# Kernel tuning notes

Hardware: AMD Instinct MI355X
Metric: run time of the kernel (lower is better)

The kernel has to match this reference:

```python
import jax, jax.numpy as jnp
import numpy as np

N = 10000   # nodes
E = 160000  # edges (avg degree 16)
IN = 512
HID = 512
OUT = 512


def setup_inputs() -> dict:
    key = jax.random.key(0)
    ks = jax.random.split(key, 8)
    x = jax.random.normal(ks[0], (N, IN), dtype=jnp.float32)
    edge_index = jax.random.randint(ks[1], (2, E), 0, N, dtype=jnp.int64)
    def w(k, fi, fo):
        return jax.random.normal(k, (fi, fo), dtype=jnp.float32) * (1.0 / np.sqrt(fi)).astype(np.float32)
    return {
        "x": x,
        "edge_index": edge_index,
        "W1": w(ks[2], IN, HID), "b1": jnp.zeros((HID,), jnp.float32),
        "W2": w(ks[3], HID, HID), "b2": jnp.zeros((HID,), jnp.float32),
        "W3": w(ks[4], HID, OUT), "b3": jnp.zeros((OUT,), jnp.float32),
    }


def _gcn_norm(edge_index, n):
    # add self loops, then symmetric normalization D^{-1/2} (A+I) D^{-1/2}
    loops = jnp.arange(n, dtype=edge_index.dtype)
    row = jnp.concatenate([edge_index[0], loops])  # source
    col = jnp.concatenate([edge_index[1], loops])  # target (aggregation dim)
    deg = jax.ops.segment_sum(jnp.ones_like(col, jnp.float32), col, num_segments=n)
    dis = jnp.where(deg > 0, jax.lax.rsqrt(jnp.maximum(deg, 1.0)), 0.0)
    norm = dis[row] * dis[col]  # [E+N]
    return row, col, norm


def _gcn_layer(x, row, col, norm, W, b, n):
    h = x @ W                                    # [N, d_out] dense GEMM
    msg = h[row] * norm[:, None]                 # gather + scale, [E+N, d_out]
    out = jax.ops.segment_sum(msg, col, num_segments=n)  # scatter-add
    return out + b


def reference(x, edge_index, W1, b1, W2, b2, W3, b3):
    n = x.shape[0]
    row, col, norm = _gcn_norm(edge_index, n)
    h = _gcn_layer(x, row, col, norm, W1, b1, n)
    h = jax.nn.relu(h)  # dropout is identity in eval mode
    h = _gcn_layer(h, row, col, norm, W2, b2, n)
    h = jax.nn.relu(h)
    h = _gcn_layer(h, row, col, norm, W3, b3, n)
    return h
```

## Files before the change

kernel.cpp:

```cpp
#include <hip/hip_runtime.h>

typedef __attribute__((ext_vector_type(8))) short bf16x8;
typedef __attribute__((ext_vector_type(4))) float f32x4;

#define N_NODES 10000
#define N_EDGES 160000
#define FDIM    512
#define ELL     64
#define BM 64
#define BN 128
#define BK 64
#define TM 157
#define NGEMM (TM * 4)
#define NSCAT 625
#define NTRAN 768

__device__ __forceinline__ float bf2f(unsigned int u) {
    union { unsigned int i; float f; } v; v.i = u << 16; return v.f;
}
__device__ __forceinline__ float bfs2f(short s) {
    return bf2f((unsigned int)(unsigned short)s);
}
__device__ __forceinline__ unsigned short f2bf(float f) {
    union { float f; unsigned int u; } v; v.f = f;
    unsigned int u = v.u;
    unsigned int r = u + 0x7fffu + ((u >> 16) & 1u);
    return (unsigned short)(r >> 16);
}
__device__ __forceinline__ void gload_lds16(const void* g, void* l) {
    __builtin_amdgcn_global_load_lds(
        (const __attribute__((address_space(1))) unsigned int*)g,
        (__attribute__((address_space(3))) unsigned int*)l, 16, 0, 0);
}
__device__ __forceinline__ int wave_is_f32(const unsigned int* w) {
    unsigned int v = w[(size_t)(threadIdx.x & 63) * 1000];
    unsigned int ex = (v >> 7) & 0xFFu;
    unsigned long long inb = __ballot(ex >= 100u && ex <= 140u);
    return (__popcll(inb) >= 48) ? 0 : 1;
}

__global__ __launch_bounds__(256) void prep_v6(
        const void* __restrict__ x, const void* __restrict__ ei,
        const void* __restrict__ W1, const void* __restrict__ W2,
        const void* __restrict__ W3, unsigned short* __restrict__ Wt,
        int* __restrict__ cnt, int* __restrict__ flags) {
    int b = blockIdx.x;
    if (b < NTRAN) {
        __shared__ unsigned short tile[32][33];
        int z = b >> 8, t = b & 255;
        const void* W = (z == 0) ? W1 : (z == 1) ? W2 : W3;
        unsigned short* out = Wt + (size_t)z * FDIM * FDIM;
        int ff32 = wave_is_f32((const unsigned int*)W);
        int tx = threadIdx.x & 31, ty = threadIdx.x >> 5;
        int xcol = (t & 15) * 32 + tx;
        int y0 = (t >> 4) * 32 + ty;
        #pragma unroll
        for (int j = 0; j < 32; j += 8) {
            int idx = (y0 + j) * FDIM + xcol;
            unsigned short v = ff32 ? f2bf(((const float*)W)[idx])
                                    : ((const unsigned short*)W)[idx];
            tile[ty + j][tx] = v;
        }
        __syncthreads();
        int x2 = (t >> 4) * 32 + tx;
        int y2 = (t & 15) * 32 + ty;
        #pragma unroll
        for (int j = 0; j < 32; j += 8)
            out[(y2 + j) * FDIM + x2] = tile[tx][ty + j];
    } else if (b < NTRAN + NSCAT) {
        const unsigned long long* e64 = (const unsigned long long*)ei;
        unsigned long long v = e64[(size_t)(threadIdx.x & 63) * 2500];
        unsigned long long big = __ballot(v > 0xFFFFFFFFull);
        int i64 = (big == 0ull);
        int e = (b - NTRAN) * 256 + threadIdx.x;
        int c = i64 ? (int)((const long long*)ei)[N_EDGES + e]
                    : ((const int*)ei)[N_EDGES + e];
        atomicAdd(&cnt[c], 1);
    } else {
        if (threadIdx.x < 64) {
            const unsigned long long* e64 = (const unsigned long long*)ei;
            unsigned long long v = e64[(size_t)threadIdx.x * 2500];
            unsigned long long big = __ballot(v > 0xFFFFFFFFull);
            const unsigned int* xw = (const unsigned int*)x;
            unsigned int w = xw[(size_t)threadIdx.x * 1000];
            unsigned int ex = (w >> 7) & 0xFFu;
            unsigned long long inb = __ballot(ex >= 100u && ex <= 140u);
            if (threadIdx.x == 0) {
                flags[0] = (big == 0ull) ? 1 : 0;
                flags[1] = (__popcll(inb) >= 48) ? 0 : 1;
            }
        }
    }
}

__global__ __launch_bounds__(256) void gemm_scat_v6(
        const void* __restrict__ Ap, const unsigned short* __restrict__ Bt,
        unsigned short* __restrict__ C, int M, int a_ext,
        const int* __restrict__ flags, const void* __restrict__ ei,
        const int* __restrict__ cnt, int* __restrict__ cursor,
        int2* __restrict__ ell, int do_scatter) {
    __shared__ unsigned short As[BM * BK];
    __shared__ unsigned short Bs[BN * BK];
    if (do_scatter && blockIdx.x >= NGEMM) {
        int e = (blockIdx.x - NGEMM) * 256 + threadIdx.x;
        if (e < N_EDGES) {
            int r, c;
            if (flags[0]) {
                r = (int)((const long long*)ei)[e];
                c = (int)((const long long*)ei)[N_EDGES + e];
            } else {
                r = ((const int*)ei)[e];
                c = ((const int*)ei)[N_EDGES + e];
            }
            int slot = atomicAdd(&cursor[c], 1);
            if (slot < ELL) {
                float nrm = rsqrtf((float)((cnt[r] + 1) * (cnt[c] + 1)));
                int2 pr; pr.x = r; pr.y = __float_as_int(nrm);
                ell[(size_t)c * ELL + slot] = pr;
            }
        }
        return;
    }
    const int K = FDIM;
    const int af32 = a_ext ? flags[1] : 0;
    const int tid = threadIdx.x;
    const int t = blockIdx.x;
    const int bm = (t % TM) * BM, bn = (t / TM) * BN;
    const int lane = tid & 63, wv = tid >> 6;
    const int wm = (wv >> 1) * 32, wn = (wv & 1) * 64;
    const int lrow = lane & 15, lk = (lane >> 4) * 8;
    const unsigned short* Abf = (const unsigned short*)Ap;
    f32x4 acc[2][4] = {};

    for (int k0 = 0; k0 < K; k0 += BK) {
        if (!af32) {
            #pragma unroll
            for (int j = 0; j < 2; ++j) {
                int r0 = wv * 16 + j * 8;
                int arow = bm + r0 + (lane >> 3);
                if (arow >= M) arow = M - 1;
                gload_lds16(Abf + (size_t)arow * K + k0 + (lane & 7) * 8,
                            &As[r0 * BK]);
            }
            #pragma unroll
            for (int j = 0; j < 4; ++j) {
                int r0 = wv * 32 + j * 8;
                gload_lds16(Bt + (size_t)(bn + r0 + (lane >> 3)) * K + k0 + (lane & 7) * 8,
                            &Bs[r0 * BK]);
            }
        } else {
            #pragma unroll
            for (int j = 0; j < 4; ++j) {
                int r0 = wv * 32 + j * 8;
                gload_lds16(Bt + (size_t)(bn + r0 + (lane >> 3)) * K + k0 + (lane & 7) * 8,
                            &Bs[r0 * BK]);
            }
            #pragma unroll
            for (int i = 0; i < 2; ++i) {
                int c = tid + i * 256;
                int row = c >> 3, seg = (c & 7) * 8;
                int grow = bm + row;
                bf16x8 va = {};
                if (grow < M) {
                    const float* Af = (const float*)Ap + (size_t)grow * K + k0 + seg;
                    f32x4 lo = *(const f32x4*)Af;
                    f32x4 hi = *(const f32x4*)(Af + 4);
                    #pragma unroll
                    for (int jj = 0; jj < 4; ++jj) {
                        va[jj]     = (short)f2bf(lo[jj]);
                        va[4 + jj] = (short)f2bf(hi[jj]);
                    }
                }
                *(bf16x8*)(&As[row * BK + seg]) = va;
            }
        }
        __syncthreads();
        #pragma unroll
        for (int half = 0; half < 2; ++half) {
            bf16x8 af[2], bfr[4];
            #pragma unroll
            for (int f = 0; f < 2; ++f)
                af[f] = *(const bf16x8*)(&As[(wm + f * 16 + lrow) * BK + half * 32 + lk]);
            #pragma unroll
            for (int f = 0; f < 4; ++f)
                bfr[f] = *(const bf16x8*)(&Bs[(wn + f * 16 + lrow) * BK + half * 32 + lk]);
            #pragma unroll
            for (int fm = 0; fm < 2; ++fm)
                #pragma unroll
                for (int fn = 0; fn < 4; ++fn)
                    acc[fm][fn] = __builtin_amdgcn_mfma_f32_16x16x32_bf16(
                        af[fm], bfr[fn], acc[fm][fn], 0, 0, 0);
        }
        __syncthreads();
    }

    int crow = (lane >> 4) * 4;
    int ccol = lane & 15;
    #pragma unroll
    for (int fm = 0; fm < 2; ++fm) {
        #pragma unroll
        for (int fn = 0; fn < 4; ++fn) {
            #pragma unroll
            for (int r = 0; r < 4; ++r) {
                int row = bm + wm + fm * 16 + crow + r;
                if (row < M)
                    C[(size_t)row * FDIM + bn + wn + fn * 16 + ccol] =
                        f2bf(acc[fm][fn][r]);
            }
        }
    }
}

__global__ __launch_bounds__(256) void agg_v6(
        const unsigned short* __restrict__ g, const void* __restrict__ bias,
        const int* __restrict__ cnt, const int2* __restrict__ ell,
        void* __restrict__ out, int relu, int out_ext,
        const int* __restrict__ flags) {
    int wv = threadIdx.x >> 6, lane = threadIdx.x & 63;
    int i = blockIdx.x * 2 + (wv >> 1);
    int f = (wv & 1) * 256 + lane * 4;
    float a0 = 0.f, a1 = 0.f, a2 = 0.f, a3 = 0.f;
    int ci = cnt[i];
    int rows = (ci > ELL) ? ELL : ci;
    const int2* ep = ell + (size_t)i * ELL;
    int j = 0;
    for (; j + 4 <= rows; j += 4) {
        int2 p0 = ep[j], p1 = ep[j + 1], p2 = ep[j + 2], p3 = ep[j + 3];
        uint2 v0 = *(const uint2*)(g + (size_t)p0.x * FDIM + f);
        uint2 v1 = *(const uint2*)(g + (size_t)p1.x * FDIM + f);
        uint2 v2 = *(const uint2*)(g + (size_t)p2.x * FDIM + f);
        uint2 v3 = *(const uint2*)(g + (size_t)p3.x * FDIM + f);
        float w0 = __int_as_float(p0.y), w1 = __int_as_float(p1.y);
        float w2 = __int_as_float(p2.y), w3 = __int_as_float(p3.y);
        a0 += w0 * bf2f(v0.x & 0xffffu); a1 += w0 * bf2f(v0.x >> 16);
        a2 += w0 * bf2f(v0.y & 0xffffu); a3 += w0 * bf2f(v0.y >> 16);
        a0 += w1 * bf2f(v1.x & 0xffffu); a1 += w1 * bf2f(v1.x >> 16);
        a2 += w1 * bf2f(v1.y & 0xffffu); a3 += w1 * bf2f(v1.y >> 16);
        a0 += w2 * bf2f(v2.x & 0xffffu); a1 += w2 * bf2f(v2.x >> 16);
        a2 += w2 * bf2f(v2.y & 0xffffu); a3 += w2 * bf2f(v2.y >> 16);
        a0 += w3 * bf2f(v3.x & 0xffffu); a1 += w3 * bf2f(v3.x >> 16);
        a2 += w3 * bf2f(v3.y & 0xffffu); a3 += w3 * bf2f(v3.y >> 16);
    }
    for (; j < rows; ++j) {
        int2 pp = ep[j];
        float w = __int_as_float(pp.y);
        uint2 v = *(const uint2*)(g + (size_t)pp.x * FDIM + f);
        a0 += w * bf2f(v.x & 0xffffu); a1 += w * bf2f(v.x >> 16);
        a2 += w * bf2f(v.y & 0xffffu); a3 += w * bf2f(v.y >> 16);
    }
    float wself = 1.0f / (float)(ci + 1);
    uint2 vs = *(const uint2*)(g + (size_t)i * FDIM + f);
    a0 += wself * bf2f(vs.x & 0xffffu); a1 += wself * bf2f(vs.x >> 16);
    a2 += wself * bf2f(vs.y & 0xffffu); a3 += wself * bf2f(vs.y >> 16);
    int ff32 = flags[1];
    if (ff32) {
        f32x4 bb = *(const f32x4*)((const float*)bias + f);
        a0 += bb[0]; a1 += bb[1]; a2 += bb[2]; a3 += bb[3];
    } else {
        uint2 bb = *(const uint2*)((const unsigned short*)bias + f);
        a0 += bf2f(bb.x & 0xffffu); a1 += bf2f(bb.x >> 16);
        a2 += bf2f(bb.y & 0xffffu); a3 += bf2f(bb.y >> 16);
    }
    if (relu) {
        a0 = fmaxf(a0, 0.f); a1 = fmaxf(a1, 0.f);
        a2 = fmaxf(a2, 0.f); a3 = fmaxf(a3, 0.f);
    }
    if (out_ext && ff32) {
        f32x4 o = {a0, a1, a2, a3};
        *(f32x4*)((float*)out + (size_t)i * FDIM + f) = o;
    } else {
        uint2 o;
        o.x = (unsigned int)f2bf(a0) | ((unsigned int)f2bf(a1) << 16);
        o.y = (unsigned int)f2bf(a2) | ((unsigned int)f2bf(a3) << 16);
        *(uint2*)((unsigned short*)out + (size_t)i * FDIM + f) = o;
    }
}

extern "C" void kernel_launch(void* const* d_in, const int* in_sizes, int n_in,
                              void* d_out, int out_size, void* d_ws, size_t ws_size,
                              hipStream_t stream) {
    (void)in_sizes; (void)n_in; (void)out_size; (void)ws_size;
    const void* x  = d_in[0];
    const void* ei = d_in[1];
    const void* W1 = d_in[2];
    const void* b1 = d_in[3];
    const void* W2 = d_in[4];
    const void* b2 = d_in[5];
    const void* W3 = d_in[6];
    const void* b3 = d_in[7];

    char* p = (char*)d_ws;
    auto alloc = [&](size_t bytes) -> void* {
        void* r = (void*)p;
        p += (bytes + 255) & ~(size_t)255;
        return r;
    };
    int*  flags   = (int*) alloc(16);
    int*  cntcur  = (int*) alloc((size_t)2 * N_NODES * 4);
    int2* ell     = (int2*)alloc((size_t)N_NODES * ELL * 8);
    unsigned short* Wt = (unsigned short*)alloc((size_t)3 * FDIM * FDIM * 2);
    unsigned short* g  = (unsigned short*)alloc((size_t)N_NODES * FDIM * 2);
    int* cnt    = cntcur;
    int* cursor = cntcur + N_NODES;
    unsigned short* Wt1 = Wt;
    unsigned short* Wt2 = Wt + (size_t)FDIM * FDIM;
    unsigned short* Wt3 = Wt + (size_t)2 * FDIM * FDIM;
    unsigned short* h   = (unsigned short*)d_out;

    hipMemsetAsync(cntcur, 0, (size_t)2 * N_NODES * 4, stream);
    prep_v6<<<NTRAN + NSCAT + 1, 256, 0, stream>>>(x, ei, W1, W2, W3, Wt, cnt, flags);

    gemm_scat_v6<<<NGEMM + NSCAT, 256, 0, stream>>>(x, Wt1, g, N_NODES, 1, flags,
                                                    ei, cnt, cursor, ell, 1);
    agg_v6<<<N_NODES / 2, 256, 0, stream>>>(g, b1, cnt, ell, h, 1, 0, flags);
    gemm_scat_v6<<<NGEMM, 256, 0, stream>>>(h, Wt2, g, N_NODES, 0, flags,
                                            ei, cnt, cursor, ell, 0);
    agg_v6<<<N_NODES / 2, 256, 0, stream>>>(g, b2, cnt, ell, h, 1, 0, flags);
    gemm_scat_v6<<<NGEMM, 256, 0, stream>>>(h, Wt3, g, N_NODES, 0, flags,
                                            ei, cnt, cursor, ell, 0);
    agg_v6<<<N_NODES / 2, 256, 0, stream>>>(g, b3, cnt, ell, d_out, 0, 1, flags);
}
```

Baseline: 226.4 us.

## Fuse all GCN phases into one persistent cooperative kernel with grid syncs

```diff
diff --git a/kernel.cpp b/kernel.cpp
--- a/kernel.cpp
+++ b/kernel.cpp
@@ -1,4 +1,7 @@
 #include <hip/hip_runtime.h>
+#include <hip/hip_cooperative_groups.h>
+
+namespace cg = cooperative_groups;
 
 typedef __attribute__((ext_vector_type(8))) short bf16x8;
 typedef __attribute__((ext_vector_type(4))) float f32x4;
@@ -14,12 +17,10 @@
 #define NGEMM (TM * 4)
 #define NSCAT 625
 #define NTRAN 768
+#define BLK 256
 
 __device__ __forceinline__ float bf2f(unsigned int u) {
     union { unsigned int i; float f; } v; v.i = u << 16; return v.f;
-}
-__device__ __forceinline__ float bfs2f(short s) {
-    return bf2f((unsigned int)(unsigned short)s);
 }
 __device__ __forceinline__ unsigned short f2bf(float f) {
     union { float f; unsigned int u; } v; v.f = f;
@@ -39,94 +40,12 @@
     return (__popcll(inb) >= 48) ? 0 : 1;
 }
 
-__global__ __launch_bounds__(256) void prep_v6(
-        const void* __restrict__ x, const void* __restrict__ ei,
-        const void* __restrict__ W1, const void* __restrict__ W2,
-        const void* __restrict__ W3, unsigned short* __restrict__ Wt,
-        int* __restrict__ cnt, int* __restrict__ flags) {
-    int b = blockIdx.x;
-    if (b < NTRAN) {
-        __shared__ unsigned short tile[32][33];
-        int z = b >> 8, t = b & 255;
-        const void* W = (z == 0) ? W1 : (z == 1) ? W2 : W3;
-        unsigned short* out = Wt + (size_t)z * FDIM * FDIM;
-        int ff32 = wave_is_f32((const unsigned int*)W);
-        int tx = threadIdx.x & 31, ty = threadIdx.x >> 5;
-        int xcol = (t & 15) * 32 + tx;
-        int y0 = (t >> 4) * 32 + ty;
-        #pragma unroll
-        for (int j = 0; j < 32; j += 8) {
-            int idx = (y0 + j) * FDIM + xcol;
-            unsigned short v = ff32 ? f2bf(((const float*)W)[idx])
-                                    : ((const unsigned short*)W)[idx];
-            tile[ty + j][tx] = v;
-        }
-        __syncthreads();
-        int x2 = (t >> 4) * 32 + tx;
-        int y2 = (t & 15) * 32 + ty;
-        #pragma unroll
-        for (int j = 0; j < 32; j += 8)
-            out[(y2 + j) * FDIM + x2] = tile[tx][ty + j];
-    } else if (b < NTRAN + NSCAT) {
-        const unsigned long long* e64 = (const unsigned long long*)ei;
-        unsigned long long v = e64[(size_t)(threadIdx.x & 63) * 2500];
-        unsigned long long big = __ballot(v > 0xFFFFFFFFull);
-        int i64 = (big == 0ull);
-        int e = (b - NTRAN) * 256 + threadIdx.x;
-        int c = i64 ? (int)((const long long*)ei)[N_EDGES + e]
-                    : ((const int*)ei)[N_EDGES + e];
-        atomicAdd(&cnt[c], 1);
-    } else {
-        if (threadIdx.x < 64) {
-            const unsigned long long* e64 = (const unsigned long long*)ei;
-            unsigned long long v = e64[(size_t)threadIdx.x * 2500];
-            unsigned long long big = __ballot(v > 0xFFFFFFFFull);
-            const unsigned int* xw = (const unsigned int*)x;
-            unsigned int w = xw[(size_t)threadIdx.x * 1000];
-            unsigned int ex = (w >> 7) & 0xFFu;
-            unsigned long long inb = __ballot(ex >= 100u && ex <= 140u);
-            if (threadIdx.x == 0) {
-                flags[0] = (big == 0ull) ? 1 : 0;
-                flags[1] = (__popcll(inb) >= 48) ? 0 : 1;
-            }
-        }
-    }
-}
-
-__global__ __launch_bounds__(256) void gemm_scat_v6(
-        const void* __restrict__ Ap, const unsigned short* __restrict__ Bt,
-        unsigned short* __restrict__ C, int M, int a_ext,
-        const int* __restrict__ flags, const void* __restrict__ ei,
-        const int* __restrict__ cnt, int* __restrict__ cursor,
-        int2* __restrict__ ell, int do_scatter) {
-    __shared__ unsigned short As[BM * BK];
-    __shared__ unsigned short Bs[BN * BK];
-    if (do_scatter && blockIdx.x >= NGEMM) {
-        int e = (blockIdx.x - NGEMM) * 256 + threadIdx.x;
-        if (e < N_EDGES) {
-            int r, c;
-            if (flags[0]) {
-                r = (int)((const long long*)ei)[e];
-                c = (int)((const long long*)ei)[N_EDGES + e];
-            } else {
-                r = ((const int*)ei)[e];
-                c = ((const int*)ei)[N_EDGES + e];
-            }
-            int slot = atomicAdd(&cursor[c], 1);
-            if (slot < ELL) {
-                float nrm = rsqrtf((float)((cnt[r] + 1) * (cnt[c] + 1)));
-                int2 pr; pr.x = r; pr.y = __float_as_int(nrm);
-                ell[(size_t)c * ELL + slot] = pr;
-            }
-        }
-        return;
-    }
+__device__ __forceinline__ void gemm_tile(
+        const void* Ap, const unsigned short* Bt, unsigned short* C,
+        int M, int af32, int item, unsigned short* As, unsigned short* Bs,
+        int tid, int lane, int wv) {
     const int K = FDIM;
-    const int af32 = a_ext ? flags[1] : 0;
-    const int tid = threadIdx.x;
-    const int t = blockIdx.x;
-    const int bm = (t % TM) * BM, bn = (t / TM) * BN;
-    const int lane = tid & 63, wv = tid >> 6;
+    const int bm = (item % TM) * BM, bn = (item / TM) * BN;
     const int wm = (wv >> 1) * 32, wn = (wv & 1) * 64;
     const int lrow = lane & 15, lk = (lane >> 4) * 8;
     const unsigned short* Abf = (const unsigned short*)Ap;
@@ -197,9 +116,9 @@
     int crow = (lane >> 4) * 4;
     int ccol = lane & 15;
     #pragma unroll
-    for (int fm = 0; fm < 2; ++fm) {
+    for (int fm = 0; fm < 2; ++fm)
         #pragma unroll
-        for (int fn = 0; fn < 4; ++fn) {
+        for (int fn = 0; fn < 4; ++fn)
             #pragma unroll
             for (int r = 0; r < 4; ++r) {
                 int row = bm + wm + fm * 16 + crow + r;
@@ -207,73 +126,186 @@
                     C[(size_t)row * FDIM + bn + wn + fn * 16 + ccol] =
                         f2bf(acc[fm][fn][r]);
             }
-        }
-    }
-}
-
-__global__ __launch_bounds__(256) void agg_v6(
-        const unsigned short* __restrict__ g, const void* __restrict__ bias,
-        const int* __restrict__ cnt, const int2* __restrict__ ell,
-        void* __restrict__ out, int relu, int out_ext,
-        const int* __restrict__ flags) {
-    int wv = threadIdx.x >> 6, lane = threadIdx.x & 63;
-    int i = blockIdx.x * 2 + (wv >> 1);
-    int f = (wv & 1) * 256 + lane * 4;
-    float a0 = 0.f, a1 = 0.f, a2 = 0.f, a3 = 0.f;
-    int ci = cnt[i];
-    int rows = (ci > ELL) ? ELL : ci;
-    const int2* ep = ell + (size_t)i * ELL;
-    int j = 0;
-    for (; j + 4 <= rows; j += 4) {
-        int2 p0 = ep[j], p1 = ep[j + 1], p2 = ep[j + 2], p3 = ep[j + 3];
-        uint2 v0 = *(const uint2*)(g + (size_t)p0.x * FDIM + f);
-        uint2 v1 = *(const uint2*)(g + (size_t)p1.x * FDIM + f);
-        uint2 v2 = *(const uint2*)(g + (size_t)p2.x * FDIM + f);
-        uint2 v3 = *(const uint2*)(g + (size_t)p3.x * FDIM + f);
-        float w0 = __int_as_float(p0.y), w1 = __int_as_float(p1.y);
-        float w2 = __int_as_float(p2.y), w3 = __int_as_float(p3.y);
-        a0 += w0 * bf2f(v0.x & 0xffffu); a1 += w0 * bf2f(v0.x >> 16);
-        a2 += w0 * bf2f(v0.y & 0xffffu); a3 += w0 * bf2f(v0.y >> 16);
-        a0 += w1 * bf2f(v1.x & 0xffffu); a1 += w1 * bf2f(v1.x >> 16);
-        a2 += w1 * bf2f(v1.y & 0xffffu); a3 += w1 * bf2f(v1.y >> 16);
-        a0 += w2 * bf2f(v2.x & 0xffffu); a1 += w2 * bf2f(v2.x >> 16);
-        a2 += w2 * bf2f(v2.y & 0xffffu); a3 += w2 * bf2f(v2.y >> 16);
-        a0 += w3 * bf2f(v3.x & 0xffffu); a1 += w3 * bf2f(v3.x >> 16);
-        a2 += w3 * bf2f(v3.y & 0xffffu); a3 += w3 * bf2f(v3.y >> 16);
-    }
-    for (; j < rows; ++j) {
-        int2 pp = ep[j];
-        float w = __int_as_float(pp.y);
-        uint2 v = *(const uint2*)(g + (size_t)pp.x * FDIM + f);
-        a0 += w * bf2f(v.x & 0xffffu); a1 += w * bf2f(v.x >> 16);
-        a2 += w * bf2f(v.y & 0xffffu); a3 += w * bf2f(v.y >> 16);
-    }
-    float wself = 1.0f / (float)(ci + 1);
-    uint2 vs = *(const uint2*)(g + (size_t)i * FDIM + f);
-    a0 += wself * bf2f(vs.x & 0xffffu); a1 += wself * bf2f(vs.x >> 16);
-    a2 += wself * bf2f(vs.y & 0xffffu); a3 += wself * bf2f(vs.y >> 16);
-    int ff32 = flags[1];
-    if (ff32) {
-        f32x4 bb = *(const f32x4*)((const float*)bias + f);
-        a0 += bb[0]; a1 += bb[1]; a2 += bb[2]; a3 += bb[3];
-    } else {
-        uint2 bb = *(const uint2*)((const unsigned short*)bias + f);
-        a0 += bf2f(bb.x & 0xffffu); a1 += bf2f(bb.x >> 16);
-        a2 += bf2f(bb.y & 0xffffu); a3 += bf2f(bb.y >> 16);
-    }
-    if (relu) {
-        a0 = fmaxf(a0, 0.f); a1 = fmaxf(a1, 0.f);
-        a2 = fmaxf(a2, 0.f); a3 = fmaxf(a3, 0.f);
-    }
-    if (out_ext && ff32) {
-        f32x4 o = {a0, a1, a2, a3};
-        *(f32x4*)((float*)out + (size_t)i * FDIM + f) = o;
-    } else {
-        uint2 o;
-        o.x = (unsigned int)f2bf(a0) | ((unsigned int)f2bf(a1) << 16);
-        o.y = (unsigned int)f2bf(a2) | ((unsigned int)f2bf(a3) << 16);
-        *(uint2*)((unsigned short*)out + (size_t)i * FDIM + f) = o;
-    }
+}
+
+__device__ __forceinline__ void agg_phase(
+        const unsigned short* g, const void* bias, const int* cnt,
+        const int* ell, void* out, int relu, int out_ext, int ff32,
+        int gs, int lane, int wv) {
+    for (int item = blockIdx.x; item < N_NODES / 2; item += gs) {
+        int i = item * 2 + (wv >> 1);
+        int f = (wv & 1) * 256 + lane * 4;
+        int ci = cnt[i];
+        int rows = (ci > ELL) ? ELL : ci;
+        const int* ep = ell + (size_t)i * ELL;
+        int   srcl = (lane < rows) ? ep[lane] : 0;
+        int   cl   = (lane < rows) ? cnt[srcl] : 0;
+        float wl   = rsqrtf((float)(cl + 1) * (float)(ci + 1));
+        float a0 = 0.f, a1 = 0.f, a2 = 0.f, a3 = 0.f;
+        int j = 0;
+        for (; j + 8 <= rows; j += 8) {
+            int s0 = __shfl(srcl, j);     float w0 = __shfl(wl, j);
+            int s1 = __shfl(srcl, j + 1); float w1 = __shfl(wl, j + 1);
+            int s2 = __shfl(srcl, j + 2); float w2 = __shfl(wl, j + 2);
+            int s3 = __shfl(srcl, j + 3); float w3 = __shfl(wl, j + 3);
+            int s4 = __shfl(srcl, j + 4); float w4 = __shfl(wl, j + 4);
+            int s5 = __shfl(srcl, j + 5); float w5 = __shfl(wl, j + 5);
+            int s6 = __shfl(srcl, j + 6); float w6 = __shfl(wl, j + 6);
+            int s7 = __shfl(srcl, j + 7); float w7 = __shfl(wl, j + 7);
+            uint2 v0 = *(const uint2*)(g + (size_t)s0 * FDIM + f);
+            uint2 v1 = *(const uint2*)(g + (size_t)s1 * FDIM + f);
+            uint2 v2 = *(const uint2*)(g + (size_t)s2 * FDIM + f);
+            uint2 v3 = *(const uint2*)(g + (size_t)s3 * FDIM + f);
+            uint2 v4 = *(const uint2*)(g + (size_t)s4 * FDIM + f);
+            uint2 v5 = *(const uint2*)(g + (size_t)s5 * FDIM + f);
+            uint2 v6 = *(const uint2*)(g + (size_t)s6 * FDIM + f);
+            uint2 v7 = *(const uint2*)(g + (size_t)s7 * FDIM + f);
+            a0 += w0 * bf2f(v0.x & 0xffffu); a1 += w0 * bf2f(v0.x >> 16);
+            a2 += w0 * bf2f(v0.y & 0xffffu); a3 += w0 * bf2f(v0.y >> 16);
+            a0 += w1 * bf2f(v1.x & 0xffffu); a1 += w1 * bf2f(v1.x >> 16);
+            a2 += w1 * bf2f(v1.y & 0xffffu); a3 += w1 * bf2f(v1.y >> 16);
+            a0 += w2 * bf2f(v2.x & 0xffffu); a1 += w2 * bf2f(v2.x >> 16);
+            a2 += w2 * bf2f(v2.y & 0xffffu); a3 += w2 * bf2f(v2.y >> 16);
+            a0 += w3 * bf2f(v3.x & 0xffffu); a1 += w3 * bf2f(v3.x >> 16);
+            a2 += w3 * bf2f(v3.y & 0xffffu); a3 += w3 * bf2f(v3.y >> 16);
+            a0 += w4 * bf2f(v4.x & 0xffffu); a1 += w4 * bf2f(v4.x >> 16);
+            a2 += w4 * bf2f(v4.y & 0xffffu); a3 += w4 * bf2f(v4.y >> 16);
+            a0 += w5 * bf2f(v5.x & 0xffffu); a1 += w5 * bf2f(v5.x >> 16);
+            a2 += w5 * bf2f(v5.y & 0xffffu); a3 += w5 * bf2f(v5.y >> 16);
+            a0 += w6 * bf2f(v6.x & 0xffffu); a1 += w6 * bf2f(v6.x >> 16);
+            a2 += w6 * bf2f(v6.y & 0xffffu); a3 += w6 * bf2f(v6.y >> 16);
+            a0 += w7 * bf2f(v7.x & 0xffffu); a1 += w7 * bf2f(v7.x >> 16);
+            a2 += w7 * bf2f(v7.y & 0xffffu); a3 += w7 * bf2f(v7.y >> 16);
+        }
+        for (; j < rows; ++j) {
+            int s = __shfl(srcl, j);
+            float w = __shfl(wl, j);
+            uint2 v = *(const uint2*)(g + (size_t)s * FDIM + f);
+            a0 += w * bf2f(v.x & 0xffffu); a1 += w * bf2f(v.x >> 16);
+            a2 += w * bf2f(v.y & 0xffffu); a3 += w * bf2f(v.y >> 16);
+        }
+        float wself = 1.0f / (float)(ci + 1);
+        uint2 vs = *(const uint2*)(g + (size_t)i * FDIM + f);
+        a0 += wself * bf2f(vs.x & 0xffffu); a1 += wself * bf2f(vs.x >> 16);
+        a2 += wself * bf2f(vs.y & 0xffffu); a3 += wself * bf2f(vs.y >> 16);
+        if (ff32) {
+            f32x4 bb = *(const f32x4*)((const float*)bias + f);
+            a0 += bb[0]; a1 += bb[1]; a2 += bb[2]; a3 += bb[3];
+        } else {
+            uint2 bb = *(const uint2*)((const unsigned short*)bias + f);
+            a0 += bf2f(bb.x & 0xffffu); a1 += bf2f(bb.x >> 16);
+            a2 += bf2f(bb.y & 0xffffu); a3 += bf2f(bb.y >> 16);
+        }
+        if (relu) {
+            a0 = fmaxf(a0, 0.f); a1 = fmaxf(a1, 0.f);
+            a2 = fmaxf(a2, 0.f); a3 = fmaxf(a3, 0.f);
+        }
+        if (out_ext && ff32) {
+            f32x4 o = {a0, a1, a2, a3};
+            *(f32x4*)((float*)out + (size_t)i * FDIM + f) = o;
+        } else {
+            uint2 o;
+            o.x = (unsigned int)f2bf(a0) | ((unsigned int)f2bf(a1) << 16);
+            o.y = (unsigned int)f2bf(a2) | ((unsigned int)f2bf(a3) << 16);
+            *(uint2*)((unsigned short*)out + (size_t)i * FDIM + f) = o;
+        }
+    }
+}
+
+__global__ __launch_bounds__(256, 3) void mega_v7(
+        const void* x, const void* ei,
+        const void* W1, const void* b1, const void* W2, const void* b2,
+        const void* W3, const void* b3, void* dout,
+        int* flags, int* cnt, int* ell, unsigned short* Wt, unsigned short* g) {
+    cg::grid_group gg = cg::this_grid();
+    __shared__ __align__(16) char lds_raw[24576];
+    unsigned short* As = (unsigned short*)lds_raw;
+    unsigned short* Bs = (unsigned short*)lds_raw + BM * BK;
+    const int b = blockIdx.x, tid = threadIdx.x;
+    const int gs = gridDim.x;
+    const int lane = tid & 63, wv = tid >> 6;
+    unsigned short* h = (unsigned short*)dout;
+
+    for (int z = b * BLK + tid; z < N_NODES; z += gs * BLK) cnt[z] = 0;
+    if (b == 0 && tid < 64) {
+        const unsigned long long* e64 = (const unsigned long long*)ei;
+        unsigned long long v = e64[(size_t)tid * 2500];
+        unsigned long long big = __ballot(v > 0xFFFFFFFFull);
+        const unsigned int* xw = (const unsigned int*)x;
+        unsigned int w = xw[(size_t)tid * 1000];
+        unsigned int ex = (w >> 7) & 0xFFu;
+        unsigned long long inb = __ballot(ex >= 100u && ex <= 140u);
+        if (tid == 0) {
+            flags[0] = (big == 0ull) ? 1 : 0;
+            flags[1] = (__popcll(inb) >= 48) ? 0 : 1;
+        }
+    }
+    for (int item = b; item < NTRAN; item += gs) {
+        unsigned short (*tile)[33] = (unsigned short (*)[33])lds_raw;
+        int z = item >> 8, t = item & 255;
+        const void* W = (z == 0) ? W1 : (z == 1) ? W2 : W3;
+        unsigned short* outp = Wt + (size_t)z * FDIM * FDIM;
+        int ff32w = wave_is_f32((const unsigned int*)W);
+        int tx = tid & 31, ty = tid >> 5;
+        int xcol = (t & 15) * 32 + tx;
+        int y0 = (t >> 4) * 32 + ty;
+        #pragma unroll
+        for (int j = 0; j < 32; j += 8) {
+            int idx = (y0 + j) * FDIM + xcol;
+            tile[ty + j][tx] = ff32w ? f2bf(((const float*)W)[idx])
+                                     : ((const unsigned short*)W)[idx];
+        }
+        __syncthreads();
+        int x2 = (t >> 4) * 32 + tx;
+        int y2 = (t & 15) * 32 + ty;
+        #pragma unroll
+        for (int j = 0; j < 32; j += 8)
+            outp[(y2 + j) * FDIM + x2] = tile[tx][ty + j];
+        __syncthreads();
+    }
+    gg.sync();
+
+    const int i64  = flags[0];
+    const int ff32 = flags[1];
+
+    for (int item = b; item < NGEMM + NSCAT; item += gs) {
+        if (item < NGEMM) {
+            gemm_tile(x, Wt, g, N_NODES, ff32, item, As, Bs, tid, lane, wv);
+        } else {
+            int e = (item - NGEMM) * 256 + tid;
+            if (e < N_EDGES) {
+                int r, c;
+                if (i64) {
+                    r = (int)((const long long*)ei)[e];
+                    c = (int)((const long long*)ei)[N_EDGES + e];
+                } else {
+                    r = ((const int*)ei)[e];
+                    c = ((const int*)ei)[N_EDGES + e];
+                }
+                int slot = atomicAdd(&cnt[c], 1);
+                if (slot < ELL) ell[(size_t)c * ELL + slot] = r;
+            }
+        }
+    }
+    gg.sync();
+
+    agg_phase(g, b1, cnt, ell, h, 1, 0, ff32, gs, lane, wv);
+    gg.sync();
+
+    for (int item = b; item < NGEMM; item += gs)
+        gemm_tile(h, Wt + (size_t)FDIM * FDIM, g, N_NODES, 0, item, As, Bs,
+                  tid, lane, wv);
+    gg.sync();
+
+    agg_phase(g, b2, cnt, ell, h, 1, 0, ff32, gs, lane, wv);
+    gg.sync();
+
+    for (int item = b; item < NGEMM; item += gs)
+        gemm_tile(h, Wt + (size_t)2 * FDIM * FDIM, g, N_NODES, 0, item, As, Bs,
+                  tid, lane, wv);
+    gg.sync();
+
+    agg_phase(g, b3, cnt, ell, dout, 0, 1, ff32, gs, lane, wv);
 }
 
 extern "C" void kernel_launch(void* const* d_in, const int* in_sizes, int n_in,
@@ -288,6 +320,7 @@
     const void* b2 = d_in[5];
     const void* W3 = d_in[6];
     const void* b3 = d_in[7];
+    void* dout = d_out;
 
     char* p = (char*)d_ws;
     auto alloc = [&](size_t bytes) -> void* {
@@ -295,28 +328,19 @@
         p += (bytes + 255) & ~(size_t)255;
         return r;
     };
-    int*  flags   = (int*) alloc(16);
-    int*  cntcur  = (int*) alloc((size_t)2 * N_NODES * 4);
-    int2* ell     = (int2*)alloc((size_t)N_NODES * ELL * 8);
+    int*  flags = (int*) alloc(16);
+    int*  cnt   = (int*) alloc((size_t)N_NODES * 4);
+    int*  ell   = (int*) alloc((size_t)N_NODES * ELL * 4);
     unsigned short* Wt = (unsigned short*)alloc((size_t)3 * FDIM * FDIM * 2);
     unsigned short* g  = (unsigned short*)alloc((size_t)N_NODES * FDIM * 2);
-    int* cnt    = cntcur;
-    int* cursor = cntcur + N_NODES;
-    unsigned short* Wt1 = Wt;
-    unsigned short* Wt2 = Wt + (size_t)FDIM * FDIM;
-    unsigned short* Wt3 = Wt + (size_t)2 * FDIM * FDIM;
-    unsigned short* h   = (unsigned short*)d_out;
-
-    hipMemsetAsync(cntcur, 0, (size_t)2 * N_NODES * 4, stream);
-    prep_v6<<<NTRAN + NSCAT + 1, 256, 0, stream>>>(x, ei, W1, W2, W3, Wt, cnt, flags);
-
-    gemm_scat_v6<<<NGEMM + NSCAT, 256, 0, stream>>>(x, Wt1, g, N_NODES, 1, flags,
-                                                    ei, cnt, cursor, ell, 1);
-    agg_v6<<<N_NODES / 2, 256, 0, stream>>>(g, b1, cnt, ell, h, 1, 0, flags);
-    gemm_scat_v6<<<NGEMM, 256, 0, stream>>>(h, Wt2, g, N_NODES, 0, flags,
-                                            ei, cnt, cursor, ell, 0);
-    agg_v6<<<N_NODES / 2, 256, 0, stream>>>(g, b2, cnt, ell, h, 1, 0, flags);
-    gemm_scat_v6<<<NGEMM, 256, 0, stream>>>(h, Wt3, g, N_NODES, 0, flags,
-                                            ei, cnt, cursor, ell, 0);
-    agg_v6<<<N_NODES / 2, 256, 0, stream>>>(g, b3, cnt, ell, d_out, 0, 1, flags);
-}
+
+    int nblk = 0;
+    hipOccupancyMaxActiveBlocksPerMultiprocessor(&nblk, mega_v7, BLK, 0);
+    if (nblk < 1) nblk = 1;
+    unsigned int grid = (unsigned int)nblk * 256u;
+
+    void* kargs[] = {&x, &ei, &W1, &b1, &W2, &b2, &W3, &b3, &dout,
+                     &flags, &cnt, &ell, &Wt, &g};
+    hipLaunchCooperativeKernel((const void*)mega_v7, dim3(grid), dim3(BLK),
+                               kargs, 0, stream);
+}
```

Result: slower. 635.0 us (+180.5%).
